# Kernel tuning notes

Hardware: AMD Instinct MI355X
Metric: run time of the kernel (lower is better)

Reference implementation:

```python
import jax, jax.numpy as jnp
import numpy as np

EPS = 1e-8
LEAK = 0.2


def upsample_linear_2x(x):
    # PyTorch nn.Upsample(scale_factor=2, mode='linear', align_corners=False) on [B,C,L]
    B, C, L = x.shape
    Lo = 2 * L
    coords = jnp.maximum((jnp.arange(Lo, dtype=jnp.float32) + 0.5) / 2.0 - 0.5, 0.0)
    i0 = jnp.minimum(jnp.floor(coords).astype(jnp.int32), L - 1)
    i1 = jnp.minimum(i0 + 1, L - 1)
    w = (coords - i0.astype(jnp.float32)).astype(x.dtype)
    return x[..., i0] * (1.0 - w) + x[..., i1] * w


def mod_conv1d(x, style, W, demod=True):
    # Style-modulated conv (StyleGAN2 Conv2DMod adapted to 1D).
    # x: [B,C,L], style: [B,C], W: [F,C,K]. Equivalent to per-sample weight
    # W*(style+1) (optionally demodulated) via input scaling + shared conv.
    s = style + 1.0
    pad = (W.shape[-1] - 1) // 2
    y = jax.lax.conv_general_dilated(x * s[:, :, None], W, (1,), [(pad, pad)],
                                     dimension_numbers=('NCH', 'OIH', 'NCH'))
    if demod:
        wmod = W[None] * s[:, None, :, None]              # [B,F,C,K]
        d = jax.lax.rsqrt(jnp.sum(wmod * wmod, axis=(2, 3)) + EPS)  # [B,F]
        y = y * d[:, :, None]
    return y


def setup_inputs() -> dict:
    key = jax.random.key(0)
    ks = jax.random.split(key, 12)
    B, Cin, F, L, Z = 8, 256, 128, 2048, 256
    Lu = 2 * L
    inp = {}
    inp['x'] = jax.random.normal(ks[0], (B, Cin, L), jnp.float32)
    inp['prev_rgb'] = jax.random.normal(ks[1], (B, 1, Lu), jnp.float32)
    inp['istyle'] = jax.random.normal(ks[2], (B, Z), jnp.float32)
    inp['inoise'] = jax.random.normal(ks[3], (B, 100), jnp.float32)
    # learned parameters
    inp['style1_w'] = jax.random.normal(ks[4], (Cin, Z), jnp.float32) * 0.02
    inp['style1_b'] = jnp.zeros((Cin,), jnp.float32)
    inp['conv1_w'] = jax.random.normal(ks[5], (F, Cin, 3), jnp.float32) * 0.05
    inp['noise_w1'] = jax.random.normal(ks[6], (F * Lu, 100), jnp.float32) * 0.01
    inp['style2_w'] = jax.random.normal(ks[7], (F, Z), jnp.float32) * 0.02
    inp['style2_b'] = jnp.zeros((F,), jnp.float32)
    inp['conv2_w'] = jax.random.normal(ks[8], (F, F, 3), jnp.float32) * 0.05
    inp['noise_w2'] = jax.random.normal(ks[9], (F * Lu, 100), jnp.float32) * 0.01
    inp['rgb_style_w'] = jax.random.normal(ks[10], (F, Z), jnp.float32) * 0.02
    inp['rgb_style_b'] = jnp.zeros((F,), jnp.float32)
    inp['rgb_conv_w'] = jax.random.normal(ks[11], (1, F, 1), jnp.float32) * 0.05
    return inp


def reference(x, prev_rgb, istyle, inoise, style1_w, style1_b, conv1_w, noise_w1,
              style2_w, style2_b, conv2_w, noise_w2, rgb_style_w, rgb_style_b, rgb_conv_w):
    x = upsample_linear_2x(x)                                 # [B,Cin,Lu]
    s1 = istyle @ style1_w.T + style1_b                       # [B,Cin]
    x = mod_conv1d(x, s1, conv1_w, demod=True)                # [B,F,Lu]
    n1 = (inoise @ noise_w1.T).reshape(x.shape)               # noise injection 1
    x = jax.nn.leaky_relu(x + n1, LEAK)
    s2 = istyle @ style2_w.T + style2_b                       # [B,F]
    x = mod_conv1d(x, s2, conv2_w, demod=True)                # [B,F,Lu]
    n2 = (inoise @ noise_w2.T).reshape(x.shape)               # noise injection 2
    x = jax.nn.leaky_relu(x + n2, LEAK)
    srgb = istyle @ rgb_style_w.T + rgb_style_b               # [B,F]
    rgb = jnp.einsum('bcl,fc->bfl', x * (srgb + 1.0)[:, :, None], rgb_conv_w[:, :, 0])
    rgb = rgb + prev_rgb
    rgb = upsample_linear_2x(rgb)                             # [B,1,2*Lu]
    return (x, rgb)
```

## Files before the change

### kernel.cpp

```cpp
#include <hip/hip_runtime.h>
#include <hip/hip_bf16.h>

#define EPS 1e-8f
#define LEAK 0.2f

#define B 8
#define CIN 256
#define F 128
#define L 2048
#define LU 4096
#define Z 256
#define NZ 100
#define S (F * LU)

typedef __attribute__((ext_vector_type(8))) short bf16x8;
typedef __attribute__((ext_vector_type(4))) float f32x4;

__device__ inline unsigned short f2bf(float x) {
    unsigned u = __builtin_bit_cast(unsigned, x);
    u += 0x7fffu + ((u >> 16) & 1u);
    return (unsigned short)(u >> 16);
}
__device__ inline float bf2f(unsigned short h) {
    unsigned u = ((unsigned)h) << 16;
    return __builtin_bit_cast(float, u);
}
__device__ inline void gload_lds16(const void* g, void* l) {
    __builtin_amdgcn_global_load_lds((const __attribute__((address_space(1))) void*)g,
                                     (__attribute__((address_space(3))) void*)l, 16, 0, 0);
}

__global__ void k_styles(const float* __restrict__ istyle,
                         const float* __restrict__ s1w, const float* __restrict__ s1b,
                         const float* __restrict__ s2w, const float* __restrict__ s2b,
                         const float* __restrict__ rgbw, const float* __restrict__ rgbb,
                         const float* __restrict__ rgbcw,
                         const float* __restrict__ W1, const float* __restrict__ W2,
                         float* __restrict__ s1, float* __restrict__ s2,
                         float* __restrict__ srgbS,
                         float* __restrict__ d1, float* __restrict__ d2,
                         unsigned short* __restrict__ Wt1, unsigned short* __restrict__ Wt2) {
    int t = threadIdx.x;
    {
        int i = blockIdx.x * 256 + t;
        if (i < 3 * F * CIN) {
            int kk = i / (F * CIN);
            int rem = i - kk * (F * CIN);
            int f = rem >> 8, c = rem & 255;
            Wt1[i] = f2bf(W1[(f * CIN + c) * 3 + kk]);
        }
        if (i < 3 * F * F) {
            int kk = i / (F * F);
            int rem = i - kk * (F * F);
            int f = rem >> 7, c = rem & 127;
            Wt2[i] = f2bf(W2[(f * F + c) * 3 + kk]);
        }
    }
    if (blockIdx.x >= 8) return;
    __shared__ float is[Z];
    __shared__ float sh1[CIN];
    __shared__ float sh2[F];
    int b = blockIdx.x;
    if (t < Z) is[t] = istyle[b * Z + t];
    __syncthreads();
    {
        float acc = 0.f;
        const float* w = s1w + (size_t)t * Z;
        for (int z = 0; z < Z; z += 4) {
            float4 v = *(const float4*)(w + z);
            acc += v.x * is[z] + v.y * is[z + 1] + v.z * is[z + 2] + v.w * is[z + 3];
        }
        float v = acc + s1b[t] + 1.0f;
        sh1[t] = v;
        s1[b * CIN + t] = v;
    }
    if (t < F) {
        float a2 = 0.f, a3 = 0.f;
        const float* w2 = s2w + (size_t)t * Z;
        const float* w3 = rgbw + (size_t)t * Z;
        for (int z = 0; z < Z; z += 4) {
            float4 u2 = *(const float4*)(w2 + z);
            float4 u3 = *(const float4*)(w3 + z);
            a2 += u2.x * is[z] + u2.y * is[z + 1] + u2.z * is[z + 2] + u2.w * is[z + 3];
            a3 += u3.x * is[z] + u3.y * is[z + 1] + u3.z * is[z + 2] + u3.w * is[z + 3];
        }
        float v2 = a2 + s2b[t] + 1.0f;
        sh2[t] = v2;
        s2[b * F + t] = v2;
        srgbS[b * F + t] = (a3 + rgbb[t] + 1.0f) * rgbcw[t];
    }
    __syncthreads();
    if (t < F) {
        float acc = 0.f;
        const float* w = W1 + (size_t)t * CIN * 3;
        for (int c = 0; c < CIN; c += 4) {
            float4 va = *(const float4*)(w + c * 3);
            float4 vb = *(const float4*)(w + c * 3 + 4);
            float4 vc = *(const float4*)(w + c * 3 + 8);
            float s0 = sh1[c], s1v = sh1[c + 1], s2v = sh1[c + 2], s3 = sh1[c + 3];
            acc += s0 * s0 * (va.x * va.x + va.y * va.y + va.z * va.z);
            acc += s1v * s1v * (va.w * va.w + vb.x * vb.x + vb.y * vb.y);
            acc += s2v * s2v * (vb.z * vb.z + vb.w * vb.w + vc.x * vc.x);
            acc += s3 * s3 * (vc.y * vc.y + vc.z * vc.z + vc.w * vc.w);
        }
        d1[b * F + t] = rsqrtf(acc + EPS);
    } else {
        int f = t - F;
        float acc = 0.f;
        const float* w = W2 + (size_t)f * F * 3;
        for (int c = 0; c < F; c += 4) {
            float4 va = *(const float4*)(w + c * 3);
            float4 vb = *(const float4*)(w + c * 3 + 4);
            float4 vc = *(const float4*)(w + c * 3 + 8);
            float s0 = sh2[c], s1v = sh2[c + 1], s2v = sh2[c + 2], s3 = sh2[c + 3];
            acc += s0 * s0 * (va.x * va.x + va.y * va.y + va.z * va.z);
            acc += s1v * s1v * (va.w * va.w + vb.x * vb.x + vb.y * vb.y);
            acc += s2v * s2v * (vb.z * vb.z + vb.w * vb.w + vc.x * vc.x);
            acc += s3 * s3 * (vc.y * vc.y + vc.z * vc.z + vc.w * vc.w);
        }
        d2[b * F + f] = rsqrtf(acc + EPS);
    }
}

__global__ __launch_bounds__(256) void k_prepx(const float* __restrict__ x,
                                               const float* __restrict__ s1,
                                               unsigned short* __restrict__ xt) {
    int b = blockIdx.z, c0 = blockIdx.y * 64, l0 = blockIdx.x * 64;
    int t = threadIdx.x;
    __shared__ float xj[64][37];
    int j0 = (l0 >> 1) - 1;
    for (int idx = t; idx < 64 * 34; idx += 256) {
        int c = idx / 34, jj = idx - c * 34;
        int j = j0 + jj;
        j = j < 0 ? 0 : (j > L - 1 ? L - 1 : j);
        xj[c][jj] = x[((size_t)(b * CIN + c0 + c)) * L + j];
    }
    __syncthreads();
    int c = t & 63;
    int lg = t >> 6;
    float s = s1[b * CIN + c0 + c];
    for (int li = 0; li < 16; ++li) {
        int ll = lg * 16 + li;
        int l = l0 + ll;
        int j = l >> 1;
        int jj = j - j0;
        float v;
        if (l & 1) {
            v = 0.75f * xj[c][jj] + 0.25f * xj[c][jj + 1];
        } else {
            v = (j == 0) ? xj[c][jj] : (0.25f * xj[c][jj - 1] + 0.75f * xj[c][jj]);
        }
        xt[((size_t)(b * LU + l)) * CIN + c0 + c] = f2bf(v * s);
    }
}

__global__ __launch_bounds__(256) void k_conv1(const unsigned short* __restrict__ xt,
                                               const unsigned short* __restrict__ Wt1,
                                               const float* __restrict__ d1,
                                               unsigned short* __restrict__ y1) {
    const int b0 = blockIdx.y * 2;
    const int l0 = blockIdx.x * 64;
    const int nfb = blockIdx.z * 4;
    const int lane = threadIdx.x & 63, wv = threadIdx.x >> 6;
    const int lbase = l0 + wv * 16;
    const int m = lane & 15, ks = lane >> 4;

    f32x4 acc[2][4];
#pragma unroll
    for (int bb = 0; bb < 2; ++bb)
#pragma unroll
        for (int nf = 0; nf < 4; ++nf) acc[bb][nf] = (f32x4)0.f;

    const unsigned short* xb0 = xt + ((size_t)(b0 + 0) * LU) * CIN + ks * 8;
    const unsigned short* xb1 = xt + ((size_t)(b0 + 1) * LU) * CIN + ks * 8;

#pragma unroll 2
    for (int kc = 0; kc < 8; ++kc) {
#pragma unroll
        for (int kk = 0; kk < 3; ++kk) {
            int lA = lbase + m + kk - 1;
            bf16x8 a0 = (bf16x8)0, a1 = (bf16x8)0;
            if (lA >= 0 && lA < LU) {
                a0 = *(const bf16x8*)&xb0[(size_t)lA * CIN + kc * 32];
                a1 = *(const bf16x8*)&xb1[(size_t)lA * CIN + kc * 32];
            }
#pragma unroll
            for (int nf = 0; nf < 4; ++nf) {
                const bf16x8 w =
                    *(const bf16x8*)&Wt1[((kk * F + (nfb + nf) * 16 + m) << 8) + kc * 32 + ks * 8];
                acc[0][nf] = __builtin_amdgcn_mfma_f32_16x16x32_bf16(a0, w, acc[0][nf], 0, 0, 0);
                acc[1][nf] = __builtin_amdgcn_mfma_f32_16x16x32_bf16(a1, w, acc[1][nf], 0, 0, 0);
            }
        }
    }
#pragma unroll
    for (int bb = 0; bb < 2; ++bb) {
        int b = b0 + bb;
#pragma unroll
        for (int nf = 0; nf < 4; ++nf) {
            int f = (nfb + nf) * 16 + m;
            float dm = d1[b * F + f];
#pragma unroll
            for (int q = 0; q < 4; ++q) {
                int l = lbase + ks * 4 + q;
                y1[((size_t)(b * LU + l) << 7) + f] = f2bf(acc[bb][nf][q] * dm);
            }
        }
    }
}

__global__ __launch_bounds__(256) void k_noise1(unsigned short* y1,
                                                const float* __restrict__ nw,
                                                const float* __restrict__ inoise,
                                                const float* __restrict__ s2) {
    __shared__ float lds[2][6400];
    const int t = threadIdx.x;
    const int rr = t & 63;
    const int b0 = (t >> 6) * 2;
    const float* inb = inoise + __builtin_amdgcn_readfirstlane(b0) * NZ;
    const int f0 = (blockIdx.x >> 8) * 32;
    const int l0 = (blockIdx.x & 255) * 16;
    const int fseg = rr >> 1, dl = rr & 1;
    const int f = f0 + fseg;

    const float s2v0 = s2[b0 * F + f];
    const float s2v1 = s2[(b0 + 1) * F + f];
    unsigned short yv0[8], yv1[8];
#pragma unroll
    for (int cc = 0; cc < 8; ++cc) {
        int l = l0 + 2 * cc + dl;
        size_t i = (size_t)l * F + f;
        yv0[cc] = y1[(size_t)b0 * S + i];
        yv1[cc] = y1[(size_t)(b0 + 1) * S + i];
    }

    auto stage = [&](int buf, int cc) {
        const int lbase = l0 + 2 * cc;
#pragma unroll
        for (int r = 0; r < 7; ++r) {
            int g = r * 256 + t;
            if (g < 1600) {
                int fs = g / 50;
                int rem = g - fs * 50;
                int d2 = (rem >= 25) ? 1 : 0;
                int m = rem - 25 * d2;
                const float* src = nw + ((size_t)(f0 + fs) * LU + lbase + d2) * NZ + m * 4;
                gload_lds16(src, &lds[buf][g * 4]);
            }
        }
    };

    auto compute = [&](int buf, int cc) {
        const float* rp = &lds[buf][rr * 100];
        float a0 = 0.f, a1 = 0.f;
#pragma unroll
        for (int q = 0; q < 25; ++q) {
            float4 v = *(const float4*)&rp[q * 4];
            int z = q * 4;
            a0 += v.x * inb[z] + v.y * inb[z + 1] + v.z * inb[z + 2] + v.w * inb[z + 3];
            a1 += v.x * inb[NZ + z] + v.y * inb[NZ + z + 1] + v.z * inb[NZ + z + 2] +
                  v.w * inb[NZ + z + 3];
        }
        const int l = l0 + 2 * cc + dl;
        const size_t i = (size_t)l * F + f;
        float val0 = bf2f(yv0[cc]) + a0;
        val0 = val0 >= 0.f ? val0 : LEAK * val0;
        y1[(size_t)b0 * S + i] = f2bf(val0 * s2v0);
        float val1 = bf2f(yv1[cc]) + a1;
        val1 = val1 >= 0.f ? val1 : LEAK * val1;
        y1[(size_t)(b0 + 1) * S + i] = f2bf(val1 * s2v1);
    };

    stage(0, 0);
    __syncthreads();
#pragma unroll
    for (int cc = 0; cc < 8; ++cc) {
        if (cc < 7) stage((cc + 1) & 1, cc + 1);
        compute(cc & 1, cc);
        __syncthreads();
    }
}

__global__ __launch_bounds__(256) void k_conv2(const unsigned short* __restrict__ y1n,
                                               const unsigned short* __restrict__ Wt2,
                                               const float* __restrict__ d2,
                                               float* __restrict__ xout) {
    const int b0 = blockIdx.y * 2;
    const int l0 = blockIdx.x * 64;
    const int mfb = blockIdx.z * 4;
    const int lane = threadIdx.x & 63, wv = threadIdx.x >> 6;
    const int lbase = l0 + wv * 16;
    const int m = lane & 15, ks = lane >> 4;

    f32x4 acc[2][4];
#pragma unroll
    for (int bb = 0; bb < 2; ++bb)
#pragma unroll
        for (int mf = 0; mf < 4; ++mf) acc[bb][mf] = (f32x4)0.f;

    const unsigned short* yb0 = y1n + ((size_t)(b0 + 0) * LU) * F + ks * 8;
    const unsigned short* yb1 = y1n + ((size_t)(b0 + 1) * LU) * F + ks * 8;

#pragma unroll 2
    for (int kc = 0; kc < 4; ++kc) {
#pragma unroll
        for (int kk = 0; kk < 3; ++kk) {
            int lB = lbase + m + kk - 1;
            bf16x8 bv0 = (bf16x8)0, bv1 = (bf16x8)0;
            if (lB >= 0 && lB < LU) {
                bv0 = *(const bf16x8*)&yb0[(size_t)lB * F + kc * 32];
                bv1 = *(const bf16x8*)&yb1[(size_t)lB * F + kc * 32];
            }
#pragma unroll
            for (int mf = 0; mf < 4; ++mf) {
                const bf16x8 w =
                    *(const bf16x8*)&Wt2[((kk * F + (mfb + mf) * 16 + m) << 7) + kc * 32 + ks * 8];
                acc[0][mf] = __builtin_amdgcn_mfma_f32_16x16x32_bf16(w, bv0, acc[0][mf], 0, 0, 0);
                acc[1][mf] = __builtin_amdgcn_mfma_f32_16x16x32_bf16(w, bv1, acc[1][mf], 0, 0, 0);
            }
        }
    }
#pragma unroll
    for (int bb = 0; bb < 2; ++bb) {
        int b = b0 + bb;
#pragma unroll
        for (int mf = 0; mf < 4; ++mf) {
#pragma unroll
            for (int q = 0; q < 4; ++q) {
                int f = (mfb + mf) * 16 + ks * 4 + q;
                int l = lbase + m;
                xout[((size_t)(b * F + f) << 12) + l] = acc[bb][mf][q] * d2[b * F + f];
            }
        }
    }
}

__global__ __launch_bounds__(256) void k_noise2(const float* __restrict__ nw,
                                                const float* __restrict__ inoise,
                                                float* xio) {
    __shared__ float lds[2][6400];
    const int t = threadIdx.x;
    const int rr = t & 63;
    const int b0 = (t >> 6) * 2;
    const float* inb = inoise + __builtin_amdgcn_readfirstlane(b0) * NZ;
    const int row0 = blockIdx.x * 512;

    float xv0[8], xv1[8];
#pragma unroll
    for (int cc = 0; cc < 8; ++cc) {
        size_t i = (size_t)row0 + cc * 64 + rr;
        xv0[cc] = xio[(size_t)b0 * S + i];
        xv1[cc] = xio[(size_t)(b0 + 1) * S + i];
    }

    auto stage = [&](int buf, int cc) {
        const float* src0 = nw + ((size_t)row0 + cc * 64) * NZ;
#pragma unroll
        for (int r = 0; r < 7; ++r) {
            int g = r * 256 + t;
            if (g < 1600) gload_lds16(src0 + g * 4, &lds[buf][g * 4]);
        }
    };

    auto compute = [&](int buf, int cc) {
        const float* rp = &lds[buf][rr * 100];
        float a0 = 0.f, a1 = 0.f;
#pragma unroll
        for (int q = 0; q < 25; ++q) {
            float4 v = *(const float4*)&rp[q * 4];
            int z = q * 4;
            a0 += v.x * inb[z] + v.y * inb[z + 1] + v.z * inb[z + 2] + v.w * inb[z + 3];
            a1 += v.x * inb[NZ + z] + v.y * inb[NZ + z + 1] + v.z * inb[NZ + z + 2] +
                  v.w * inb[NZ + z + 3];
        }
        const size_t i = (size_t)row0 + cc * 64 + rr;
        float val0 = xv0[cc] + a0;
        val0 = val0 >= 0.f ? val0 : LEAK * val0;
        xio[(size_t)b0 * S + i] = val0;
        float val1 = xv1[cc] + a1;
        val1 = val1 >= 0.f ? val1 : LEAK * val1;
        xio[(size_t)(b0 + 1) * S + i] = val1;
    };

    stage(0, 0);
    __syncthreads();
#pragma unroll
    for (int cc = 0; cc < 8; ++cc) {
        if (cc < 7) stage((cc + 1) & 1, cc + 1);
        compute(cc & 1, cc);
        __syncthreads();
    }
}

__global__ __launch_bounds__(256) void k_rgb(const float* __restrict__ xf,
                                             const float* __restrict__ srgbS,
                                             const float* __restrict__ prev,
                                             float* __restrict__ rgb) {
    int b = blockIdx.y;
    int o0 = blockIdx.x * 512;
    int t = threadIdx.x;
    __shared__ float ss[F];
    __shared__ float pre[258];
    if (t < F) ss[t] = srgbS[b * F + t];
    __syncthreads();
    int j0 = (o0 >> 1) - 1;
    for (int jj = t; jj < 258; jj += 256) {
        int j = j0 + jj;
        j = j < 0 ? 0 : (j > LU - 1 ? LU - 1 : j);
        float acc = prev[b * LU + j];
        const float* xb = xf + (size_t)b * S + j;
        for (int f = 0; f < F; ++f) acc += xb[(size_t)f * LU] * ss[f];
        pre[jj] = acc;
    }
    __syncthreads();
    int jj = t + 1;
    int j = j0 + jj;
    float ve = (j == 0) ? pre[jj] : (0.25f * pre[jj - 1] + 0.75f * pre[jj]);
    float vo = 0.75f * pre[jj] + 0.25f * pre[jj + 1];
    float2 v2 = make_float2(ve, vo);
    *(float2*)&rgb[(size_t)b * 2 * LU + o0 + 2 * t] = v2;
}

extern "C" void kernel_launch(void* const* d_in, const int* in_sizes, int n_in,
                              void* d_out, int out_size, void* d_ws, size_t ws_size,
                              hipStream_t stream) {
    const float* x      = (const float*)d_in[0];
    const float* prev   = (const float*)d_in[1];
    const float* istyle = (const float*)d_in[2];
    const float* inoise = (const float*)d_in[3];
    const float* s1w    = (const float*)d_in[4];
    const float* s1b    = (const float*)d_in[5];
    const float* W1     = (const float*)d_in[6];
    const float* nw1    = (const float*)d_in[7];
    const float* s2w    = (const float*)d_in[8];
    const float* s2b    = (const float*)d_in[9];
    const float* W2     = (const float*)d_in[10];
    const float* nw2    = (const float*)d_in[11];
    const float* rgbw   = (const float*)d_in[12];
    const float* rgbb   = (const float*)d_in[13];
    const float* rgbcw  = (const float*)d_in[14];

    char* w = (char*)d_ws;
    float* s1      = (float*)(w);
    float* s2      = (float*)(w + 8 * 1024);
    float* srgbS   = (float*)(w + 12 * 1024);
    float* d1      = (float*)(w + 16 * 1024);
    float* d2      = (float*)(w + 20 * 1024);
    unsigned short* Wt1 = (unsigned short*)(w + 256 * 1024);
    unsigned short* Wt2 = (unsigned short*)(w + 448 * 1024);
    unsigned short* y1  = (unsigned short*)(w + (size_t)1024 * 1024);

    unsigned short* xt = (unsigned short*)d_out;

    float* xout   = (float*)d_out;
    float* rgbout = xout + (size_t)B * S;

    k_styles<<<384, 256, 0, stream>>>(istyle, s1w, s1b, s2w, s2b, rgbw, rgbb, rgbcw,
                                      W1, W2, s1, s2, srgbS, d1, d2, Wt1, Wt2);
    k_prepx<<<dim3(LU / 64, CIN / 64, B), 256, 0, stream>>>(x, s1, xt);
    k_conv1<<<dim3(LU / 64, B / 2, 2), 256, 0, stream>>>(xt, Wt1, d1, y1);
    k_noise1<<<1024, 256, 0, stream>>>(y1, nw1, inoise, s2);
    k_conv2<<<dim3(LU / 64, B / 2, 2), 256, 0, stream>>>(y1, Wt2, d2, xout);
    k_noise2<<<1024, 256, 0, stream>>>(nw2, inoise, xout);
    k_rgb<<<dim3(2 * LU / 512, B), 256, 0, stream>>>(xout, srgbS, prev, rgbout);
}
```

Before: 244.7 us.

## Deepen noise-kernel LDS prefetch to four stages with fine-grained vmcnt waits

Both noise-injection kernels move from a double-buffered LDS pipeline with full __syncthreads to a four-buffer pipeline that prefetches three chunks ahead. Waits use explicit s_waitcnt vmcnt counts per wave (wave 0 issues a different number of loads) plus a raw s_barrier, so more global-to-LDS loads stay in flight. This targets latency on the memory-bound noise-weight stream. It doubles LDS use to about 100KB per block, which lowers occupancy, and the hand-computed vmcnt counts are fragile and may be wrong if the compiler reorders or merges loads.

```diff
diff --git a/kernel.cpp b/kernel.cpp
--- a/kernel.cpp
+++ b/kernel.cpp
@@ -213,10 +213,11 @@
                                                 const float* __restrict__ nw,
                                                 const float* __restrict__ inoise,
                                                 const float* __restrict__ s2) {
-    __shared__ float lds[2][6400];
+    __shared__ float lds[4][6400];
     const int t = threadIdx.x;
     const int rr = t & 63;
     const int b0 = (t >> 6) * 2;
+    const bool w0 = (t >> 6) == 0;
     const float* inb = inoise + __builtin_amdgcn_readfirstlane(b0) * NZ;
     const int f0 = (blockIdx.x >> 8) * 32;
     const int l0 = (blockIdx.x & 255) * 16;
@@ -272,13 +273,25 @@
     };
 
     stage(0, 0);
-    __syncthreads();
-#pragma unroll
-    for (int cc = 0; cc < 8; ++cc) {
-        if (cc < 7) stage((cc + 1) & 1, cc + 1);
-        compute(cc & 1, cc);
-        __syncthreads();
-    }
+    stage(1, 1);
+    stage(2, 2);
+
+#define STEP(CC, BUF, N0, N1)                                               \
+    if (w0) { asm volatile("s_waitcnt vmcnt(" #N0 ")" ::: "memory"); }      \
+    else    { asm volatile("s_waitcnt vmcnt(" #N1 ")" ::: "memory"); }      \
+    __builtin_amdgcn_s_barrier();                                           \
+    __builtin_amdgcn_sched_barrier(0);                                      \
+    compute(BUF, CC);
+
+    STEP(0, 0, 14, 12) stage(3, 3);
+    STEP(1, 1, 16, 14) stage(0, 4);
+    STEP(2, 2, 16, 14) stage(1, 5);
+    STEP(3, 3, 16, 14) stage(2, 6);
+    STEP(4, 0, 16, 14) stage(3, 7);
+    STEP(5, 1, 16, 14)
+    STEP(6, 2, 9, 8)
+    STEP(7, 3, 2, 2)
+#undef STEP
 }
 
 __global__ __launch_bounds__(256) void k_conv2(const unsigned short* __restrict__ y1n,
@@ -338,10 +351,11 @@
 __global__ __launch_bounds__(256) void k_noise2(const float* __restrict__ nw,
                                                 const float* __restrict__ inoise,
                                                 float* xio) {
-    __shared__ float lds[2][6400];
+    __shared__ float lds[4][6400];
     const int t = threadIdx.x;
     const int rr = t & 63;
     const int b0 = (t >> 6) * 2;
+    const bool w0 = (t >> 6) == 0;
     const float* inb = inoise + __builtin_amdgcn_readfirstlane(b0) * NZ;
     const int row0 = blockIdx.x * 512;
 
@@ -383,13 +397,25 @@
     };
 
     stage(0, 0);
-    __syncthreads();
-#pragma unroll
-    for (int cc = 0; cc < 8; ++cc) {
-        if (cc < 7) stage((cc + 1) & 1, cc + 1);
-        compute(cc & 1, cc);
-        __syncthreads();
-    }
+    stage(1, 1);
+    stage(2, 2);
+
+#define STEP(CC, BUF, N0, N1)                                               \
+    if (w0) { asm volatile("s_waitcnt vmcnt(" #N0 ")" ::: "memory"); }      \
+    else    { asm volatile("s_waitcnt vmcnt(" #N1 ")" ::: "memory"); }      \
+    __builtin_amdgcn_s_barrier();                                           \
+    __builtin_amdgcn_sched_barrier(0);                                      \
+    compute(BUF, CC);
+
+    STEP(0, 0, 14, 12) stage(3, 3);
+    STEP(1, 1, 16, 14) stage(0, 4);
+    STEP(2, 2, 16, 14) stage(1, 5);
+    STEP(3, 3, 16, 14) stage(2, 6);
+    STEP(4, 0, 16, 14) stage(3, 7);
+    STEP(5, 1, 16, 14)
+    STEP(6, 2, 9, 8)
+    STEP(7, 3, 2, 2)
+#undef STEP
 }
 
 __global__ __launch_bounds__(256) void k_rgb(const float* __restrict__ xf,
```

New measurement: 283.7 us. 1.16x slower.

## Triple-buffer noise weight staging with explicit vmcnt waits in noise kernels

Applied to the files above, without the earlier changes.

Both noise-injection kernels now use three LDS buffers instead of two and prefetch two stages ahead. Per-wave s_waitcnt vmcnt counts plus a raw s_barrier replace __syncthreads, so outstanding global-to-LDS loads for later stages stay in flight while the current stage is computed. The aim is to hide the latency of streaming the large noise weight matrix. The cost is 50% more LDS per block (about 77KB), which may lower occupancy. The hand-tuned vmcnt values depend on exact load counts per wave and could be wrong if the compiler's instruction emission changes.

```diff
diff --git a/kernel.cpp b/kernel.cpp
--- a/kernel.cpp
+++ b/kernel.cpp
@@ -213,10 +213,11 @@
                                                 const float* __restrict__ nw,
                                                 const float* __restrict__ inoise,
                                                 const float* __restrict__ s2) {
-    __shared__ float lds[2][6400];
+    __shared__ float lds[3][6400];
     const int t = threadIdx.x;
     const int rr = t & 63;
     const int b0 = (t >> 6) * 2;
+    const bool w0 = (t >> 6) == 0;
     const float* inb = inoise + __builtin_amdgcn_readfirstlane(b0) * NZ;
     const int f0 = (blockIdx.x >> 8) * 32;
     const int l0 = (blockIdx.x & 255) * 16;
@@ -272,13 +273,23 @@
     };
 
     stage(0, 0);
-    __syncthreads();
-#pragma unroll
-    for (int cc = 0; cc < 8; ++cc) {
-        if (cc < 7) stage((cc + 1) & 1, cc + 1);
-        compute(cc & 1, cc);
-        __syncthreads();
-    }
+    stage(1, 1);
+
+#define WSTEP(N0, N1)                                                       \
+    if (w0) { asm volatile("s_waitcnt vmcnt(" #N0 ")" ::: "memory"); }      \
+    else    { asm volatile("s_waitcnt vmcnt(" #N1 ")" ::: "memory"); }      \
+    __builtin_amdgcn_s_barrier();                                           \
+    __builtin_amdgcn_sched_barrier(0);
+
+    WSTEP(7, 6)   stage(2, 2); compute(0, 0);
+    WSTEP(9, 8)   stage(0, 3); compute(1, 1);
+    WSTEP(11, 10) stage(1, 4); compute(2, 2);
+    WSTEP(11, 10) stage(2, 5); compute(0, 3);
+    WSTEP(11, 10) stage(0, 6); compute(1, 4);
+    WSTEP(11, 10) stage(1, 7); compute(2, 5);
+    WSTEP(11, 10)              compute(0, 6);
+    WSTEP(4, 4)                compute(1, 7);
+#undef WSTEP
 }
 
 __global__ __launch_bounds__(256) void k_conv2(const unsigned short* __restrict__ y1n,
@@ -338,10 +349,11 @@
 __global__ __launch_bounds__(256) void k_noise2(const float* __restrict__ nw,
                                                 const float* __restrict__ inoise,
                                                 float* xio) {
-    __shared__ float lds[2][6400];
+    __shared__ float lds[3][6400];
     const int t = threadIdx.x;
     const int rr = t & 63;
     const int b0 = (t >> 6) * 2;
+    const bool w0 = (t >> 6) == 0;
     const float* inb = inoise + __builtin_amdgcn_readfirstlane(b0) * NZ;
     const int row0 = blockIdx.x * 512;
 
@@ -383,13 +395,23 @@
     };
 
     stage(0, 0);
-    __syncthreads();
-#pragma unroll
-    for (int cc = 0; cc < 8; ++cc) {
-        if (cc < 7) stage((cc + 1) & 1, cc + 1);
-        compute(cc & 1, cc);
-        __syncthreads();
-    }
+    stage(1, 1);
+
+#define WSTEP(N0, N1)                                                       \
+    if (w0) { asm volatile("s_waitcnt vmcnt(" #N0 ")" ::: "memory"); }      \
+    else    { asm volatile("s_waitcnt vmcnt(" #N1 ")" ::: "memory"); }      \
+    __builtin_amdgcn_s_barrier();                                           \
+    __builtin_amdgcn_sched_barrier(0);
+
+    WSTEP(7, 6)   stage(2, 2); compute(0, 0);
+    WSTEP(9, 8)   stage(0, 3); compute(1, 1);
+    WSTEP(11, 10) stage(1, 4); compute(2, 2);
+    WSTEP(11, 10) stage(2, 5); compute(0, 3);
+    WSTEP(11, 10) stage(0, 6); compute(1, 4);
+    WSTEP(11, 10) stage(1, 7); compute(2, 5);
+    WSTEP(11, 10)              compute(0, 6);
+    WSTEP(4, 4)                compute(1, 7);
+#undef WSTEP
 }
 
 __global__ __launch_bounds__(256) void k_rgb(const float* __restrict__ xf,
```

Result: faster. 238.6 us (-2.5%).
